# Kernel optimization log

Measured on AMD Instinct MI355X. Metric: run time of the kernel, lower is better.

The kernel has to match this reference:

```python
import jax, jax.numpy as jnp
import numpy as np

B, S, D, H = 2, 2048, 1024, 16
DK = D // H

def setup_inputs() -> dict:
    key = jax.random.key(0)
    ks = jax.random.split(key, 8)
    query = jax.random.normal(ks[0], (B, S, D), dtype=jnp.float32)
    k_in = jax.random.normal(ks[1], (B, S, D), dtype=jnp.float32)
    v_in = jax.random.normal(ks[2], (B, S, D), dtype=jnp.float32)
    # causal mask: 1.0 where attention is disallowed (j > i), broadcastable to (B, H, S, S)
    mask = (jnp.triu(jnp.ones((S, S), dtype=jnp.float32), k=1))[None, None, :, :] * jnp.ones((B, 1, 1, 1), jnp.float32)
    scale = 0.02
    wq = jax.random.normal(ks[3], (D, D), dtype=jnp.float32) * scale
    wk = jax.random.normal(ks[4], (D, D), dtype=jnp.float32) * scale
    wv = jax.random.normal(ks[5], (D, D), dtype=jnp.float32) * scale
    wo = jax.random.normal(ks[6], (D, D), dtype=jnp.float32) * scale
    return {"query": query, "key": k_in, "value": v_in, "mask": mask,
            "wq": wq, "wk": wk, "wv": wv, "wo": wo}

def _split_heads(x):
    # (B, S, D) -> (B, H, S, DK)
    b, s, _ = x.shape
    return x.reshape(b, s, H, DK).transpose(0, 2, 1, 3)

def reference(query, key, value, mask, wq, wk, wv, wo):
    q = _split_heads(query @ wq)
    k = _split_heads(key @ wk)
    v = _split_heads(value @ wv)
    scale = jnp.sqrt(jnp.asarray(DK, jnp.float32))
    scores = jnp.einsum('bhqd,bhkd->bhqk', q, k) / scale
    scores = scores + mask * (-1e9)
    attn_weights = jax.nn.softmax(scores, axis=-1)
    context = jnp.einsum('bhqk,bhkd->bhqd', attn_weights, v)
    context = context.transpose(0, 2, 1, 3).reshape(query.shape[0], -1, D)
    output = context @ wo
    return output, attn_weights
```

## Files before the change

### kernel.cpp

```cpp
#include <hip/hip_runtime.h>
#include <hip/hip_bf16.h>

#define S_  2048
#define Bb  2
#define Hh  16
#define DKk 64
#define Dd  1024
#define BH  32

typedef __attribute__((ext_vector_type(8))) short short8;
typedef __attribute__((ext_vector_type(8))) float float8;
typedef __attribute__((ext_vector_type(4))) float f32x4;

__device__ inline float bf2f(ushort h) {
  union { uint u; float f; } c; c.u = ((uint)h) << 16; return c.f;
}
__device__ inline ushort f2bf(float f) {
  union { float f; uint u; } c; c.f = f;
  uint u = c.u;
  return (ushort)((u + 0x7fffu + ((u >> 16) & 1u)) >> 16);
}

enum { MODE_PLAIN = 0, MODE_HEADS = 1 };

__global__ void detect_k(const ushort* __restrict__ q, int* __restrict__ flag)
{
  __shared__ int cnt;
  if (threadIdx.x == 0) cnt = 0;
  __syncthreads();
  int c = 0;
  for (int i = threadIdx.x; i < 16384; i += 256)
    c += ((q[i] & 0x7F80u) == 0x7F80u) ? 1 : 0;
  atomicAdd(&cnt, c);
  __syncthreads();
  if (threadIdx.x == 0) flag[0] = (cnt > 0) ? 1 : 0;
}

__launch_bounds__(256)
__global__ void cvt_in_k(const void* __restrict__ q, const void* __restrict__ k,
                         const void* __restrict__ v, ushort* __restrict__ out,
                         const int* __restrict__ flag)
{
  const void* src = (blockIdx.y == 0) ? q : (blockIdx.y == 1) ? k : v;
  ushort* dst = out + (long)blockIdx.y * ((long)Bb * S_ * Dd);
  const long i = ((long)blockIdx.x * 256 + threadIdx.x) * 8;
  if (flag[0] != 0) {
    float8 vv = *(const float8*)((const float*)src + i);
    short8 o;
#pragma unroll
    for (int j = 0; j < 8; j++) o[j] = (short)f2bf(vv[j]);
    *(short8*)(dst + i) = o;
  } else {
    *(short8*)(dst + i) = *(const short8*)((const ushort*)src + i);
  }
}

__launch_bounds__(256)
__global__ void cvt_wT_k(const void* __restrict__ w0, const void* __restrict__ w1,
                         const void* __restrict__ w2, const void* __restrict__ w3,
                         ushort* __restrict__ out, const int* __restrict__ flag)
{
  __shared__ ushort t[64][72];
  const bool f32 = flag[0] != 0;
  const int wsel = blockIdx.z;
  const void* w = (wsel == 0) ? w0 : (wsel == 1) ? w1 : (wsel == 2) ? w2 : w3;
  ushort* op = out + (long)wsel * (Dd * Dd);
  const int k0 = blockIdx.y * 64, n0 = blockIdx.x * 64;
  const int tid = threadIdx.x;
  for (int u = tid; u < 512; u += 256) {
    int kk = u >> 3, nc = (u & 7) * 8;
    if (f32) {
      float8 vv = *(const float8*)((const float*)w + (long)(k0 + kk) * Dd + n0 + nc);
#pragma unroll
      for (int j = 0; j < 8; j++) t[nc + j][kk] = f2bf(vv[j]);
    } else {
      short8 vv = *(const short8*)((const ushort*)w + (long)(k0 + kk) * Dd + n0 + nc);
#pragma unroll
      for (int j = 0; j < 8; j++) t[nc + j][kk] = (ushort)vv[j];
    }
  }
  __syncthreads();
  for (int u = tid; u < 512; u += 256) {
    int n = u >> 3, kc = (u & 7) * 8;
    *(uint4*)&op[(long)(n0 + n) * Dd + k0 + kc] = *(const uint4*)&t[n][kc];
  }
}

__launch_bounds__(256)
__global__ void transp_k(const ushort* __restrict__ in, ushort* __restrict__ out)
{
  __shared__ ushort t[64][72];
  const int bh = blockIdx.y, s0 = blockIdx.x * 64;
  const ushort* ip = in + (long)bh * S_ * DKk;
  ushort* op = out + (long)bh * DKk * S_;
  const int tid = threadIdx.x;
  for (int u = tid; u < 512; u += 256) {
    int r = u >> 3, c0 = (u & 7) * 8;
    *(uint4*)&t[r][c0] = *(const uint4*)&ip[(long)(s0 + r) * DKk + c0];
  }
  __syncthreads();
  for (int u = tid; u < 512; u += 256) {
    int c = u >> 3, r0 = (u & 7) * 8;
    short8 o;
#pragma unroll
    for (int j = 0; j < 8; j++) o[j] = (short)t[r0 + j][c];
    *(short8*)&op[(long)c * S_ + s0 + r0] = o;
  }
}

template<int BM, int BN, int MODE, bool ADYN, bool CDYN>
__launch_bounds__(256)
__global__ void gemm_k(const void* __restrict__ A, const void* __restrict__ B,
                       void* __restrict__ C, const int* __restrict__ flag,
                       int K, int lda, int ldb, int ldc, float scale, int scaleZ,
                       long sAz, long sBz, long sCz)
{
  constexpr int SA = 40;
  __shared__ __align__(16) short As[BM * SA];
  __shared__ __align__(16) short Bs[BN * SA];

  const bool f32 = (ADYN || CDYN) && (flag[0] != 0);

  const int bx = blockIdx.x, by = blockIdx.y, z = blockIdx.z;
  const int m0 = by * BM, n0 = bx * BN;

  const ushort* Ah = (const ushort*)A + (long)z * sAz;
  const float*  Af = (const float*) A + (long)z * sAz;
  const ushort* Bh = (const ushort*)B + (long)z * sBz;

  const int tid  = threadIdx.x;
  const int wave = tid >> 6, lane = tid & 63;
  const int lrow = lane & 15, lq = lane >> 4;
  const int WM = (wave >> 1) * 64;
  const int WN = (wave & 1) * 64;

  f32x4 acc[4][4];
#pragma unroll
  for (int a = 0; a < 4; a++)
#pragma unroll
    for (int b = 0; b < 4; b++) { f32x4 zz = {0.f, 0.f, 0.f, 0.f}; acc[a][b] = zz; }

  for (int k0 = 0; k0 < K; k0 += 32) {
    for (int u = tid; u < BM * 4; u += 256) {
      int m = u >> 2, kq = u & 3;
      long idx = (long)(m0 + m) * lda + k0 + kq * 8;
      if (ADYN && f32) {
        float8 v = *(const float8*)&Af[idx];
        short8 o;
#pragma unroll
        for (int j = 0; j < 8; j++) o[j] = (short)f2bf(v[j]);
        *(short8*)&As[m * SA + kq * 8] = o;
      } else {
        *(uint4*)&As[m * SA + kq * 8] = *(const uint4*)&Ah[idx];
      }
    }
    for (int u = tid; u < BN * 4; u += 256) {
      int n = u >> 2, kq = u & 3;
      long idx = (long)(n0 + n) * ldb + k0 + kq * 8;
      *(uint4*)&Bs[n * SA + kq * 8] = *(const uint4*)&Bh[idx];
    }
    __syncthreads();

    short8 af[4], bfr[4];
#pragma unroll
    for (int mi = 0; mi < 4; mi++)
      af[mi] = *(const short8*)&As[(WM + mi * 16 + lrow) * SA + lq * 8];
#pragma unroll
    for (int ni = 0; ni < 4; ni++)
      bfr[ni] = *(const short8*)&Bs[(WN + ni * 16 + lrow) * SA + lq * 8];
#pragma unroll
    for (int mi = 0; mi < 4; mi++)
#pragma unroll
      for (int ni = 0; ni < 4; ni++)
        acc[mi][ni] = __builtin_amdgcn_mfma_f32_16x16x32_bf16(af[mi], bfr[ni], acc[mi][ni], 0, 0, 0);
    __syncthreads();
  }

  const float sc = (scaleZ < 0 || z == scaleZ) ? scale : 1.f;
#pragma unroll
  for (int mi = 0; mi < 4; mi++) {
#pragma unroll
    for (int ni = 0; ni < 4; ni++) {
#pragma unroll
      for (int r = 0; r < 4; r++) {
        int row = m0 + WM + mi * 16 + lq * 4 + r;
        int col = n0 + WN + ni * 16 + lrow;
        float val = acc[mi][ni][r] * sc;
        if (MODE == MODE_PLAIN) {
          long idx = (long)z * sCz + (long)row * ldc + col;
          if (CDYN && f32) ((float*)C)[idx] = val;
          else             ((ushort*)C)[idx] = f2bf(val);
        } else {
          int b = row >> 11, s = row & 2047;
          int h = col >> 6, c = col & 63;
          ((ushort*)C)[(long)z * sCz + (((long)(b * Hh + h) * S_) + s) * DKk + c] = f2bf(val);
        }
      }
    }
  }
}

__launch_bounds__(512)
__global__ void flash_k(const ushort* __restrict__ Qh, const ushort* __restrict__ Kh,
                        const ushort* __restrict__ Vt, void* __restrict__ outp,
                        ushort* __restrict__ ctx, const int* __restrict__ flag)
{
  __shared__ __align__(16) short KA[2][128 * 72];
  __shared__ __align__(16) short VA[2][64 * 136];
  __shared__ __align__(16) short PL[128 * 136];

  const bool f32 = flag[0] != 0;
  const int p = blockIdx.x;
  const int z = blockIdx.y;
  const int tid = threadIdx.x;
  const int wv = tid >> 6, lane = tid & 63;
  const int lrow = lane & 15, lq = lane >> 4;
  const int b = z >> 4, h = z & 15;

  const ushort* Qz = Qh + (long)z * S_ * DKk;
  const ushort* Kz = Kh + (long)z * S_ * DKk;
  const ushort* Vz = Vt + (long)z * DKk * S_;

  for (int half = 0; half < 2; half++) {
    const int qt = (half == 0) ? (15 - p) : p;
    const long pBase = (long)Bb * S_ * Dd + ((long)z * S_ + (long)qt * 128) * S_;
    float*  pF = (float*)outp + pBase;
    ushort* pH = (ushort*)outp + pBase;

    __syncthreads();
    for (int u = tid; u < 1024; u += 512) {
      int r = u >> 3, kc = u & 7;
      *(uint4*)&PL[r * 72 + kc * 8] =
          *(const uint4*)&Qz[((long)qt * 128 + r) * DKk + kc * 8];
    }
    __syncthreads();
    short8 aq[2];
#pragma unroll
    for (int ks = 0; ks < 2; ks++)
      aq[ks] = *(const short8*)&PL[(wv * 16 + lrow) * 72 + ks * 32 + lq * 8];
    __syncthreads();

    float m_s[4], l_s[4];
#pragma unroll
    for (int r = 0; r < 4; r++) { m_s[r] = -3.0e38f; l_s[r] = 0.f; }

#pragma unroll
    for (int i = 0; i < 2; i++) {
      int u = tid + i * 512; int r = u >> 3, kc = u & 7;
      *(uint4*)&KA[0][r * 72 + kc * 8] =
          *(const uint4*)&Kz[(long)r * DKk + kc * 8];
    }
    __syncthreads();
    int buf = 0;
    for (int kt = 0; kt <= qt; kt++) {
      const bool hasPre = kt < qt;
      uint4 pk0, pk1;
      if (hasPre) {
        { int u = tid;       int r = u >> 3, kc = u & 7;
          pk0 = *(const uint4*)&Kz[((long)(kt + 1) * 128 + r) * DKk + kc * 8]; }
        { int u = tid + 512; int r = u >> 3, kc = u & 7;
          pk1 = *(const uint4*)&Kz[((long)(kt + 1) * 128 + r) * DKk + kc * 8]; }
      }
      f32x4 acc[8];
#pragma unroll
      for (int a = 0; a < 8; a++) { f32x4 zz = {0.f, 0.f, 0.f, 0.f}; acc[a] = zz; }
#pragma unroll
      for (int ks = 0; ks < 2; ks++) {
        short8 bk[8];
#pragma unroll
        for (int ni = 0; ni < 8; ni++)
          bk[ni] = *(const short8*)&KA[buf][(ni * 16 + lrow) * 72 + ks * 32 + lq * 8];
#pragma unroll
        for (int ni = 0; ni < 8; ni++)
          acc[ni] = __builtin_amdgcn_mfma_f32_16x16x32_bf16(aq[ks], bk[ni], acc[ni], 0, 0, 0);
      }
      const bool diag = (kt == qt);
#pragma unroll
      for (int r = 0; r < 4; r++) {
        const int rl = wv * 16 + lq * 4 + r;
        float vmx = -3.0e38f;
#pragma unroll
        for (int ni = 0; ni < 8; ni++) {
          float x = acc[ni][r];
          if (diag && (ni * 16 + lrow) > rl) x = -3.0e38f;
          vmx = fmaxf(vmx, x);
        }
#pragma unroll
        for (int s = 1; s < 16; s <<= 1) vmx = fmaxf(vmx, __shfl_xor(vmx, s, 16));
        const float mn = fmaxf(m_s[r], vmx);
        const float corr = __expf(m_s[r] - mn);
        float sum = 0.f;
#pragma unroll
        for (int ni = 0; ni < 8; ni++) {
          float x = acc[ni][r];
          float e = (diag && (ni * 16 + lrow) > rl) ? 0.f : __expf(x - mn);
          sum += e;
        }
#pragma unroll
        for (int s = 1; s < 16; s <<= 1) sum += __shfl_xor(sum, s, 16);
        l_s[r] = l_s[r] * corr + sum;
        m_s[r] = mn;
      }
      if (hasPre) {
        { int u = tid;       int r = u >> 3, kc = u & 7;
          *(uint4*)&KA[buf ^ 1][r * 72 + kc * 8] = pk0; }
        { int u = tid + 512; int r = u >> 3, kc = u & 7;
          *(uint4*)&KA[buf ^ 1][r * 72 + kc * 8] = pk1; }
      }
      __syncthreads();
      buf ^= 1;
    }

    float linv[4];
#pragma unroll
    for (int r = 0; r < 4; r++) linv[r] = 1.f / l_s[r];

    f32x4 accO[4];
#pragma unroll
    for (int a = 0; a < 4; a++) { f32x4 zz = {0.f, 0.f, 0.f, 0.f}; accO[a] = zz; }

#pragma unroll
    for (int i = 0; i < 2; i++) {
      int u = tid + i * 512;
      { int r = u >> 3, kc = u & 7;
        *(uint4*)&KA[0][r * 72 + kc * 8] =
            *(const uint4*)&Kz[(long)r * DKk + kc * 8]; }
      { int r = u >> 4, kc = u & 15;
        *(uint4*)&VA[0][r * 136 + kc * 8] =
            *(const uint4*)&Vz[(long)r * S_ + kc * 8]; }
    }
    __syncthreads();
    buf = 0;
    for (int kt = 0; kt <= qt; kt++) {
      const bool hasPre = kt < qt;
      uint4 pk0, pk1, pv0, pv1;
      if (hasPre) {
        { int u = tid;       int r = u >> 3, kc = u & 7;
          pk0 = *(const uint4*)&Kz[((long)(kt + 1) * 128 + r) * DKk + kc * 8]; }
        { int u = tid + 512; int r = u >> 3, kc = u & 7;
          pk1 = *(const uint4*)&Kz[((long)(kt + 1) * 128 + r) * DKk + kc * 8]; }
        { int u = tid;       int r = u >> 4, kc = u & 15;
          pv0 = *(const uint4*)&Vz[(long)r * S_ + (long)(kt + 1) * 128 + kc * 8]; }
        { int u = tid + 512; int r = u >> 4, kc = u & 15;
          pv1 = *(const uint4*)&Vz[(long)r * S_ + (long)(kt + 1) * 128 + kc * 8]; }
      }
      f32x4 acc[8];
#pragma unroll
      for (int a = 0; a < 8; a++) { f32x4 zz = {0.f, 0.f, 0.f, 0.f}; acc[a] = zz; }
#pragma unroll
      for (int ks = 0; ks < 2; ks++) {
        short8 bk[8];
#pragma unroll
        for (int ni = 0; ni < 8; ni++)
          bk[ni] = *(const short8*)&KA[buf][(ni * 16 + lrow) * 72 + ks * 32 + lq * 8];
#pragma unroll
        for (int ni = 0; ni < 8; ni++)
          acc[ni] = __builtin_amdgcn_mfma_f32_16x16x32_bf16(aq[ks], bk[ni], acc[ni], 0, 0, 0);
      }
      const bool diag = (kt == qt);
#pragma unroll
      for (int ni = 0; ni < 8; ni++) {
#pragma unroll
        for (int r = 0; r < 4; r++) {
          const int rl = wv * 16 + lq * 4 + r;
          const int cl = ni * 16 + lrow;
          const float pr = (diag && cl > rl)
                               ? 0.f
                               : __expf(acc[ni][r] - m_s[r]) * linv[r];
          const ushort pb = f2bf(pr);
          const long gi = (long)rl * S_ + (long)kt * 128 + cl;
          if (f32) pF[gi] = pr;
          else     pH[gi] = pb;
          PL[rl * 136 + cl] = (short)pb;
        }
      }
#pragma unroll
      for (int ks = 0; ks < 4; ks++) {
        short8 ap = *(const short8*)&PL[(wv * 16 + lrow) * 136 + ks * 32 + lq * 8];
        short8 bv[4];
#pragma unroll
        for (int nj = 0; nj < 4; nj++)
          bv[nj] = *(const short8*)&VA[buf][(nj * 16 + lrow) * 136 + ks * 32 + lq * 8];
#pragma unroll
        for (int nj = 0; nj < 4; nj++)
          accO[nj] = __builtin_amdgcn_mfma_f32_16x16x32_bf16(ap, bv[nj], accO[nj], 0, 0, 0);
      }
      if (hasPre) {
        { int u = tid;       int r = u >> 3, kc = u & 7;
          *(uint4*)&KA[buf ^ 1][r * 72 + kc * 8] = pk0; }
        { int u = tid + 512; int r = u >> 3, kc = u & 7;
          *(uint4*)&KA[buf ^ 1][r * 72 + kc * 8] = pk1; }
        { int u = tid;       int r = u >> 4, kc = u & 15;
          *(uint4*)&VA[buf ^ 1][r * 136 + kc * 8] = pv0; }
        { int u = tid + 512; int r = u >> 4, kc = u & 15;
          *(uint4*)&VA[buf ^ 1][r * 136 + kc * 8] = pv1; }
      }
      __syncthreads();
      buf ^= 1;
    }

#pragma unroll
    for (int nj = 0; nj < 4; nj++)
#pragma unroll
      for (int r = 0; r < 4; r++) {
        int row = qt * 128 + wv * 16 + lq * 4 + r;
        int col = h * 64 + nj * 16 + lrow;
        ctx[((long)(b * S_ + row)) * Dd + col] = f2bf(accO[nj][r]);
      }

    if (qt < 15) {
      const int c0 = (qt + 1) * 128;
      if (f32) {
        const int w4 = (S_ - c0) >> 2;
        float4 zz = {0.f, 0.f, 0.f, 0.f};
        for (int u = tid; u < 128 * w4; u += 512) {
          int rr = u / w4, cc = c0 + (u % w4) * 4;
          *(float4*)&pF[(long)rr * S_ + cc] = zz;
        }
      } else {
        const int w8 = (S_ - c0) >> 3;
        uint4 zz = {0, 0, 0, 0};
        for (int u = tid; u < 128 * w8; u += 512) {
          int rr = u / w8, cc = c0 + (u % w8) * 8;
          *(uint4*)&pH[(long)rr * S_ + cc] = zz;
        }
      }
    }
  }
}

extern "C" void kernel_launch(void* const* d_in, const int* in_sizes, int n_in,
                              void* d_out, int out_size, void* d_ws, size_t ws_size,
                              hipStream_t stream)
{
  const void* query = d_in[0];
  const void* key_  = d_in[1];
  const void* value = d_in[2];
  const void* wq = d_in[4];
  const void* wk = d_in[5];
  const void* wv = d_in[6];
  const void* wo = d_in[7];

  const long NIN = (long)Bb * S_ * Dd;
  const long NW  = (long)Dd * Dd;
  const long NH  = (long)BH * S_ * DKk;

  int*    flag = (int*)d_ws;
  ushort* base = (ushort*)d_ws + 16;
  ushort* Qc   = base;
  ushort* wT   = Qc + 3 * NIN;
  ushort* Ph   = wT + 4 * NW;
  ushort* Vt   = Ph + 3 * NH;
  ushort* ctx  = Vt + NH;

  ushort* Qh = Ph;
  ushort* Kh = Ph + NH;
  ushort* Vh = Ph + 2 * NH;

  dim3 blk(256);

  detect_k<<<1, blk, 0, stream>>>((const ushort*)query, flag);

  cvt_in_k<<<dim3(2048, 3), blk, 0, stream>>>(query, key_, value, Qc, flag);
  cvt_wT_k<<<dim3(16, 16, 4), blk, 0, stream>>>(wq, wk, wv, wo, wT, flag);

  gemm_k<128,128,MODE_HEADS,false,false><<<dim3(8,32,3), blk, 0, stream>>>(
      Qc, wT, Ph, flag, 1024, 1024, 1024, 0, 0.125f, 0,
      NIN, NW, NH);

  transp_k<<<dim3(32, 32), blk, 0, stream>>>(Vh, Vt);

  flash_k<<<dim3(8, BH), dim3(512), 0, stream>>>(Qh, Kh, Vt, d_out, ctx, flag);

  gemm_k<128,128,MODE_PLAIN,false,true><<<dim3(8,32,1), blk, 0, stream>>>(
      ctx, wT + 3 * NW, d_out, flag, 1024, 1024, 1024, 1024, 1.f, -1,
      0, 0, 0);
}
```

Measured before the change: 835.1 us.

## Fuse V transpose into projection GEMM, read K/V from global, use direct-to-LDS loads

The QKV projection GEMM now writes V directly in transposed layout, which removes the separate transpose kernel. The GEMM loads tiles with global_load_lds straight into unpadded shared memory. The flash kernel now uses 256-thread blocks over 64-row halves, doubling the grid. It drops K/V shared-memory staging and double buffering in favour of direct global/L2 fragment loads, which also removes the per-tile barriers. The costs are redundant global traffic for K/V across waves and possible LDS bank conflicts from the unpadded GEMM tiles.

Result: slower. 909.9 us (+9.0%).

```diff
diff --git a/kernel.cpp b/kernel.cpp
--- a/kernel.cpp
+++ b/kernel.cpp
@@ -19,6 +19,12 @@
   union { float f; uint u; } c; c.f = f;
   uint u = c.u;
   return (ushort)((u + 0x7fffu + ((u >> 16) & 1u)) >> 16);
+}
+
+__device__ __forceinline__ void gload16(const void* g, void* l) {
+  __builtin_amdgcn_global_load_lds(
+      (const __attribute__((address_space(1))) unsigned int*)g,
+      (__attribute__((address_space(3))) unsigned int*)l, 16, 0, 0);
 }
 
 enum { MODE_PLAIN = 0, MODE_HEADS = 1 };
@@ -86,47 +92,23 @@
   }
 }
 
+template<int BM, int BN, int MODE, bool CDYN>
 __launch_bounds__(256)
-__global__ void transp_k(const ushort* __restrict__ in, ushort* __restrict__ out)
-{
-  __shared__ ushort t[64][72];
-  const int bh = blockIdx.y, s0 = blockIdx.x * 64;
-  const ushort* ip = in + (long)bh * S_ * DKk;
-  ushort* op = out + (long)bh * DKk * S_;
-  const int tid = threadIdx.x;
-  for (int u = tid; u < 512; u += 256) {
-    int r = u >> 3, c0 = (u & 7) * 8;
-    *(uint4*)&t[r][c0] = *(const uint4*)&ip[(long)(s0 + r) * DKk + c0];
-  }
-  __syncthreads();
-  for (int u = tid; u < 512; u += 256) {
-    int c = u >> 3, r0 = (u & 7) * 8;
-    short8 o;
-#pragma unroll
-    for (int j = 0; j < 8; j++) o[j] = (short)t[r0 + j][c];
-    *(short8*)&op[(long)c * S_ + s0 + r0] = o;
-  }
-}
-
-template<int BM, int BN, int MODE, bool ADYN, bool CDYN>
-__launch_bounds__(256)
-__global__ void gemm_k(const void* __restrict__ A, const void* __restrict__ B,
+__global__ void gemm_k(const ushort* __restrict__ A, const ushort* __restrict__ B,
                        void* __restrict__ C, const int* __restrict__ flag,
                        int K, int lda, int ldb, int ldc, float scale, int scaleZ,
-                       long sAz, long sBz, long sCz)
-{
-  constexpr int SA = 40;
-  __shared__ __align__(16) short As[BM * SA];
-  __shared__ __align__(16) short Bs[BN * SA];
-
-  const bool f32 = (ADYN || CDYN) && (flag[0] != 0);
+                       long sAz, long sBz, long sCz, int vtZ)
+{
+  __shared__ __align__(16) short As[BM * 32];
+  __shared__ __align__(16) short Bs[BN * 32];
+
+  const bool f32 = CDYN && (flag[0] != 0);
 
   const int bx = blockIdx.x, by = blockIdx.y, z = blockIdx.z;
   const int m0 = by * BM, n0 = bx * BN;
 
-  const ushort* Ah = (const ushort*)A + (long)z * sAz;
-  const float*  Af = (const float*) A + (long)z * sAz;
-  const ushort* Bh = (const ushort*)B + (long)z * sBz;
+  const ushort* Ah = A + (long)z * sAz;
+  const ushort* Bh = B + (long)z * sBz;
 
   const int tid  = threadIdx.x;
   const int wave = tid >> 6, lane = tid & 63;
@@ -143,31 +125,21 @@
   for (int k0 = 0; k0 < K; k0 += 32) {
     for (int u = tid; u < BM * 4; u += 256) {
       int m = u >> 2, kq = u & 3;
-      long idx = (long)(m0 + m) * lda + k0 + kq * 8;
-      if (ADYN && f32) {
-        float8 v = *(const float8*)&Af[idx];
-        short8 o;
-#pragma unroll
-        for (int j = 0; j < 8; j++) o[j] = (short)f2bf(v[j]);
-        *(short8*)&As[m * SA + kq * 8] = o;
-      } else {
-        *(uint4*)&As[m * SA + kq * 8] = *(const uint4*)&Ah[idx];
-      }
+      gload16(&Ah[(long)(m0 + m) * lda + k0 + kq * 8], &As[u * 8]);
     }
     for (int u = tid; u < BN * 4; u += 256) {
       int n = u >> 2, kq = u & 3;
-      long idx = (long)(n0 + n) * ldb + k0 + kq * 8;
-      *(uint4*)&Bs[n * SA + kq * 8] = *(const uint4*)&Bh[idx];
+      gload16(&Bh[(long)(n0 + n) * ldb + k0 + kq * 8], &Bs[u * 8]);
     }
     __syncthreads();
 
     short8 af[4], bfr[4];
 #pragma unroll
     for (int mi = 0; mi < 4; mi++)
-      af[mi] = *(const short8*)&As[(WM + mi * 16 + lrow) * SA + lq * 8];
+      af[mi] = *(const short8*)&As[(WM + mi * 16 + lrow) * 32 + lq * 8];
 #pragma unroll
     for (int ni = 0; ni < 4; ni++)
-      bfr[ni] = *(const short8*)&Bs[(WN + ni * 16 + lrow) * SA + lq * 8];
+      bfr[ni] = *(const short8*)&Bs[(WN + ni * 16 + lrow) * 32 + lq * 8];
 #pragma unroll
     for (int mi = 0; mi < 4; mi++)
 #pragma unroll
@@ -193,74 +165,59 @@
         } else {
           int b = row >> 11, s = row & 2047;
           int h = col >> 6, c = col & 63;
-          ((ushort*)C)[(long)z * sCz + (((long)(b * Hh + h) * S_) + s) * DKk + c] = f2bf(val);
-        }
-      }
-    }
-  }
-}
-
-__launch_bounds__(512)
+          if (z == vtZ)
+            ((ushort*)C)[(long)z * sCz + ((long)(b * Hh + h) * DKk + c) * S_ + s] = f2bf(val);
+          else
+            ((ushort*)C)[(long)z * sCz + (((long)(b * Hh + h) * S_) + s) * DKk + c] = f2bf(val);
+        }
+      }
+    }
+  }
+}
+
+__launch_bounds__(256)
 __global__ void flash_k(const ushort* __restrict__ Qh, const ushort* __restrict__ Kh,
                         const ushort* __restrict__ Vt, void* __restrict__ outp,
                         ushort* __restrict__ ctx, const int* __restrict__ flag)
 {
-  __shared__ __align__(16) short KA[2][128 * 72];
-  __shared__ __align__(16) short VA[2][64 * 136];
-  __shared__ __align__(16) short PL[128 * 136];
+  constexpr int PS = 152;
+  __shared__ __align__(16) short PL[64 * PS];
 
   const bool f32 = flag[0] != 0;
-  const int p = blockIdx.x;
-  const int z = blockIdx.y;
+  const int p  = blockIdx.x;
+  const int h2 = blockIdx.y;
+  const int z  = blockIdx.z;
   const int tid = threadIdx.x;
   const int wv = tid >> 6, lane = tid & 63;
   const int lrow = lane & 15, lq = lane >> 4;
+  const int rb = wv * 16;
   const int b = z >> 4, h = z & 15;
 
   const ushort* Qz = Qh + (long)z * S_ * DKk;
   const ushort* Kz = Kh + (long)z * S_ * DKk;
   const ushort* Vz = Vt + (long)z * DKk * S_;
 
+  const int kOff = lrow * DKk + lq * 8;
+  const long vOff = (long)lrow * S_ + lq * 8;
+
   for (int half = 0; half < 2; half++) {
-    const int qt = (half == 0) ? (15 - p) : p;
-    const long pBase = (long)Bb * S_ * Dd + ((long)z * S_ + (long)qt * 128) * S_;
+    const int qt = half ? p : (15 - p);
+    const int r0 = qt * 128 + h2 * 64;
+    const long pBase = (long)Bb * S_ * Dd + ((long)z * S_ + r0) * S_;
     float*  pF = (float*)outp + pBase;
     ushort* pH = (ushort*)outp + pBase;
 
-    __syncthreads();
-    for (int u = tid; u < 1024; u += 512) {
-      int r = u >> 3, kc = u & 7;
-      *(uint4*)&PL[r * 72 + kc * 8] =
-          *(const uint4*)&Qz[((long)qt * 128 + r) * DKk + kc * 8];
-    }
-    __syncthreads();
     short8 aq[2];
 #pragma unroll
     for (int ks = 0; ks < 2; ks++)
-      aq[ks] = *(const short8*)&PL[(wv * 16 + lrow) * 72 + ks * 32 + lq * 8];
-    __syncthreads();
+      aq[ks] = *(const short8*)&Qz[(long)(r0 + rb + lrow) * DKk + ks * 32 + lq * 8];
 
     float m_s[4], l_s[4];
 #pragma unroll
     for (int r = 0; r < 4; r++) { m_s[r] = -3.0e38f; l_s[r] = 0.f; }
 
-#pragma unroll
-    for (int i = 0; i < 2; i++) {
-      int u = tid + i * 512; int r = u >> 3, kc = u & 7;
-      *(uint4*)&KA[0][r * 72 + kc * 8] =
-          *(const uint4*)&Kz[(long)r * DKk + kc * 8];
-    }
-    __syncthreads();
-    int buf = 0;
     for (int kt = 0; kt <= qt; kt++) {
-      const bool hasPre = kt < qt;
-      uint4 pk0, pk1;
-      if (hasPre) {
-        { int u = tid;       int r = u >> 3, kc = u & 7;
-          pk0 = *(const uint4*)&Kz[((long)(kt + 1) * 128 + r) * DKk + kc * 8]; }
-        { int u = tid + 512; int r = u >> 3, kc = u & 7;
-          pk1 = *(const uint4*)&Kz[((long)(kt + 1) * 128 + r) * DKk + kc * 8]; }
-      }
+      const ushort* Kt = Kz + (long)kt * 128 * DKk;
       f32x4 acc[8];
 #pragma unroll
       for (int a = 0; a < 8; a++) { f32x4 zz = {0.f, 0.f, 0.f, 0.f}; acc[a] = zz; }
@@ -269,15 +226,16 @@
         short8 bk[8];
 #pragma unroll
         for (int ni = 0; ni < 8; ni++)
-          bk[ni] = *(const short8*)&KA[buf][(ni * 16 + lrow) * 72 + ks * 32 + lq * 8];
+          bk[ni] = *(const short8*)&Kt[ni * 16 * DKk + ks * 32 + kOff];
 #pragma unroll
         for (int ni = 0; ni < 8; ni++)
           acc[ni] = __builtin_amdgcn_mfma_f32_16x16x32_bf16(aq[ks], bk[ni], acc[ni], 0, 0, 0);
       }
       const bool diag = (kt == qt);
+      const int rg = h2 * 64 + rb;
 #pragma unroll
       for (int r = 0; r < 4; r++) {
-        const int rl = wv * 16 + lq * 4 + r;
+        const int rl = rg + lq * 4 + r;
         float vmx = -3.0e38f;
 #pragma unroll
         for (int ni = 0; ni < 8; ni++) {
@@ -301,14 +259,6 @@
         l_s[r] = l_s[r] * corr + sum;
         m_s[r] = mn;
       }
-      if (hasPre) {
-        { int u = tid;       int r = u >> 3, kc = u & 7;
-          *(uint4*)&KA[buf ^ 1][r * 72 + kc * 8] = pk0; }
-        { int u = tid + 512; int r = u >> 3, kc = u & 7;
-          *(uint4*)&KA[buf ^ 1][r * 72 + kc * 8] = pk1; }
-      }
-      __syncthreads();
-      buf ^= 1;
     }
 
     float linv[4];
@@ -319,31 +269,8 @@
 #pragma unroll
     for (int a = 0; a < 4; a++) { f32x4 zz = {0.f, 0.f, 0.f, 0.f}; accO[a] = zz; }
 
-#pragma unroll
-    for (int i = 0; i < 2; i++) {
-      int u = tid + i * 512;
-      { int r = u >> 3, kc = u & 7;
-        *(uint4*)&KA[0][r * 72 + kc * 8] =
-            *(const uint4*)&Kz[(long)r * DKk + kc * 8]; }
-      { int r = u >> 4, kc = u & 15;
-        *(uint4*)&VA[0][r * 136 + kc * 8] =
-            *(const uint4*)&Vz[(long)r * S_ + kc * 8]; }
-    }
-    __syncthreads();
-    buf = 0;
     for (int kt = 0; kt <= qt; kt++) {
-      const bool hasPre = kt < qt;
-      uint4 pk0, pk1, pv0, pv1;
-      if (hasPre) {
-        { int u = tid;       int r = u >> 3, kc = u & 7;
-          pk0 = *(const uint4*)&Kz[((long)(kt + 1) * 128 + r) * DKk + kc * 8]; }
-        { int u = tid + 512; int r = u >> 3, kc = u & 7;
-          pk1 = *(const uint4*)&Kz[((long)(kt + 1) * 128 + r) * DKk + kc * 8]; }
-        { int u = tid;       int r = u >> 4, kc = u & 15;
-          pv0 = *(const uint4*)&Vz[(long)r * S_ + (long)(kt + 1) * 128 + kc * 8]; }
-        { int u = tid + 512; int r = u >> 4, kc = u & 15;
-          pv1 = *(const uint4*)&Vz[(long)r * S_ + (long)(kt + 1) * 128 + kc * 8]; }
-      }
+      const ushort* Kt = Kz + (long)kt * 128 * DKk;
       f32x4 acc[8];
 #pragma unroll
       for (int a = 0; a < 8; a++) { f32x4 zz = {0.f, 0.f, 0.f, 0.f}; acc[a] = zz; }
@@ -352,58 +279,47 @@
         short8 bk[8];
 #pragma unroll
         for (int ni = 0; ni < 8; ni++)
-          bk[ni] = *(const short8*)&KA[buf][(ni * 16 + lrow) * 72 + ks * 32 + lq * 8];
+          bk[ni] = *(const short8*)&Kt[ni * 16 * DKk + ks * 32 + kOff];
 #pragma unroll
         for (int ni = 0; ni < 8; ni++)
           acc[ni] = __builtin_amdgcn_mfma_f32_16x16x32_bf16(aq[ks], bk[ni], acc[ni], 0, 0, 0);
       }
       const bool diag = (kt == qt);
+      const int rg = h2 * 64 + rb;
 #pragma unroll
       for (int ni = 0; ni < 8; ni++) {
 #pragma unroll
         for (int r = 0; r < 4; r++) {
-          const int rl = wv * 16 + lq * 4 + r;
+          const int rl = rb + lq * 4 + r;
           const int cl = ni * 16 + lrow;
-          const float pr = (diag && cl > rl)
+          const float pr = (diag && cl > (rg + lq * 4 + r))
                                ? 0.f
                                : __expf(acc[ni][r] - m_s[r]) * linv[r];
           const ushort pb = f2bf(pr);
           const long gi = (long)rl * S_ + (long)kt * 128 + cl;
           if (f32) pF[gi] = pr;
           else     pH[gi] = pb;
-          PL[rl * 136 + cl] = (short)pb;
+          PL[rl * PS + cl] = (short)pb;
         }
       }
 #pragma unroll
       for (int ks = 0; ks < 4; ks++) {
-        short8 ap = *(const short8*)&PL[(wv * 16 + lrow) * 136 + ks * 32 + lq * 8];
+        short8 ap = *(const short8*)&PL[(rb + lrow) * PS + ks * 32 + lq * 8];
         short8 bv[4];
 #pragma unroll
         for (int nj = 0; nj < 4; nj++)
-          bv[nj] = *(const short8*)&VA[buf][(nj * 16 + lrow) * 136 + ks * 32 + lq * 8];
+          bv[nj] = *(const short8*)&Vz[vOff + (long)nj * 16 * S_ + kt * 128 + ks * 32];
 #pragma unroll
         for (int nj = 0; nj < 4; nj++)
           accO[nj] = __builtin_amdgcn_mfma_f32_16x16x32_bf16(ap, bv[nj], accO[nj], 0, 0, 0);
       }
-      if (hasPre) {
-        { int u = tid;       int r = u >> 3, kc = u & 7;
-          *(uint4*)&KA[buf ^ 1][r * 72 + kc * 8] = pk0; }
-        { int u = tid + 512; int r = u >> 3, kc = u & 7;
-          *(uint4*)&KA[buf ^ 1][r * 72 + kc * 8] = pk1; }
-        { int u = tid;       int r = u >> 4, kc = u & 15;
-          *(uint4*)&VA[buf ^ 1][r * 136 + kc * 8] = pv0; }
-        { int u = tid + 512; int r = u >> 4, kc = u & 15;
-          *(uint4*)&VA[buf ^ 1][r * 136 + kc * 8] = pv1; }
-      }
-      __syncthreads();
-      buf ^= 1;
     }
 
 #pragma unroll
     for (int nj = 0; nj < 4; nj++)
 #pragma unroll
       for (int r = 0; r < 4; r++) {
-        int row = qt * 128 + wv * 16 + lq * 4 + r;
+        int row = r0 + rb + lq * 4 + r;
         int col = h * 64 + nj * 16 + lrow;
         ctx[((long)(b * S_ + row)) * Dd + col] = f2bf(accO[nj][r]);
       }
@@ -413,14 +329,14 @@
       if (f32) {
         const int w4 = (S_ - c0) >> 2;
         float4 zz = {0.f, 0.f, 0.f, 0.f};
-        for (int u = tid; u < 128 * w4; u += 512) {
+        for (int u = tid; u < 64 * w4; u += 256) {
           int rr = u / w4, cc = c0 + (u % w4) * 4;
           *(float4*)&pF[(long)rr * S_ + cc] = zz;
         }
       } else {
         const int w8 = (S_ - c0) >> 3;
         uint4 zz = {0, 0, 0, 0};
-        for (int u = tid; u < 128 * w8; u += 512) {
+        for (int u = tid; u < 64 * w8; u += 256) {
           int rr = u / w8, cc = c0 + (u % w8) * 8;
           *(uint4*)&pH[(long)rr * S_ + cc] = zz;
         }
@@ -450,12 +366,11 @@
   ushort* Qc   = base;
   ushort* wT   = Qc + 3 * NIN;
   ushort* Ph   = wT + 4 * NW;
-  ushort* Vt   = Ph + 3 * NH;
-  ushort* ctx  = Vt + NH;
+  ushort* ctx  = Ph + 3 * NH;
 
   ushort* Qh = Ph;
   ushort* Kh = Ph + NH;
-  ushort* Vh = Ph + 2 * NH;
+  ushort* Vt = Ph + 2 * NH;
 
   dim3 blk(256);
 
@@ -464,15 +379,13 @@
   cvt_in_k<<<dim3(2048, 3), blk, 0, stream>>>(query, key_, value, Qc, flag);
   cvt_wT_k<<<dim3(16, 16, 4), blk, 0, stream>>>(wq, wk, wv, wo, wT, flag);
 
-  gemm_k<128,128,MODE_HEADS,false,false><<<dim3(8,32,3), blk, 0, stream>>>(
+  gemm_k<128,128,MODE_HEADS,false><<<dim3(8,32,3), blk, 0, stream>>>(
       Qc, wT, Ph, flag, 1024, 1024, 1024, 0, 0.125f, 0,
-      NIN, NW, NH);
-
-  transp_k<<<dim3(32, 32), blk, 0, stream>>>(Vh, Vt);
-
-  flash_k<<<dim3(8, BH), dim3(512), 0, stream>>>(Qh, Kh, Vt, d_out, ctx, flag);
-
-  gemm_k<128,128,MODE_PLAIN,false,true><<<dim3(8,32,1), blk, 0, stream>>>(
+      NIN, NW, NH, 2);
+
+  flash_k<<<dim3(8, 2, BH), blk, 0, stream>>>(Qh, Kh, Vt, d_out, ctx, flag);
+
+  gemm_k<128,128,MODE_PLAIN,true><<<dim3(8,32,1), blk, 0, stream>>>(
       ctx, wT + 3 * NW, d_out, flag, 1024, 1024, 1024, 1024, 1.f, -1,
-      0, 0, 0);
-}
+      0, 0, 0, -1);
+}
```
